# Optimization experiments

Measured on AMD Instinct MI355X. Metric: run time of the kernel, lower is better.

Reference implementation:

```python
import jax, jax.numpy as jnp
import numpy as np

N, E = 50000, 800000
IN_DIM, HID, H1, H2, NCLS = 512, 64, 4, 1, 40
NEG_SLOPE = 0.2


def gat_conv(x, src, dst, W, att_src, att_dst, b, heads, ch):
    # x: [N, F_in]; W: [F_in, heads*ch]; att_*: [heads, ch]; b: [heads*ch]
    n = x.shape[0]
    h = (x @ W).reshape(n, heads, ch)                      # [N,H,C]
    a_s = jnp.einsum('nhc,hc->nh', h, att_src)             # [N,H]
    a_d = jnp.einsum('nhc,hc->nh', h, att_dst)             # [N,H]
    e = jax.nn.leaky_relu(a_s[src] + a_d[dst], NEG_SLOPE)  # [E,H]
    # segment softmax over incoming edges of each destination node
    m = jax.ops.segment_max(e, dst, num_segments=n)        # [N,H]
    ex = jnp.exp(e - m[dst])
    s = jax.ops.segment_sum(ex, dst, num_segments=n)       # [N,H]
    alpha = ex / (s[dst] + 1e-16)                          # [E,H]
    out = jax.ops.segment_sum(alpha[:, :, None] * h[src], dst, num_segments=n)
    return out.reshape(n, heads * ch) + b


def setup_inputs() -> dict:
    key = jax.random.key(0)
    ks = jax.random.split(key, 10)
    glorot = lambda k, shp: jax.random.normal(k, shp, jnp.float32) * jnp.sqrt(2.0 / (shp[0] + shp[-1]))
    return {
        'x': jax.random.normal(ks[0], (N, IN_DIM), jnp.float32),
        'edge_index': jax.random.randint(ks[1], (2, E), 0, N, jnp.int64),
        'W1': glorot(ks[2], (IN_DIM, H1 * HID)),
        'att_src1': glorot(ks[3], (H1, HID)),
        'att_dst1': glorot(ks[4], (H1, HID)),
        'b1': jnp.zeros((H1 * HID,), jnp.float32),
        'W2': glorot(ks[5], (H1 * HID, H2 * NCLS)),
        'att_src2': glorot(ks[6], (H2, NCLS)),
        'att_dst2': glorot(ks[7], (H2, NCLS)),
        'b2': jnp.zeros((H2 * NCLS,), jnp.float32),
    }


def reference(x, edge_index, W1, att_src1, att_dst1, b1, W2, att_src2, att_dst2, b2):
    n = x.shape[0]
    loops = jnp.arange(n, dtype=edge_index.dtype)
    src = jnp.concatenate([edge_index[0], loops])  # add self loops (PyG default)
    dst = jnp.concatenate([edge_index[1], loops])
    # dropout layers are identity in eval mode
    h = gat_conv(x, src, dst, W1, att_src1, att_dst1, b1, H1, HID)
    h = jax.nn.elu(h)
    out = gat_conv(h, src, dst, W2, att_src2, att_dst2, b2, H2, NCLS)
    return jax.nn.log_softmax(out, axis=1)
```

## Files before the change

### kernel.cpp

```cpp
#include <hip/hip_runtime.h>
#include <math.h>
#include <stdint.h>


typedef short bf16x8 __attribute__((ext_vector_type(8)));
typedef float f32x4  __attribute__((ext_vector_type(4)));

static __device__ __forceinline__ float leaky(float x){ return x > 0.f ? x : 0.2f*x; }
static __device__ __forceinline__ unsigned short f2bf(float f){
  uint32_t u = __float_as_uint(f);
  uint32_t r = u + 0x7fffu + ((u >> 16) & 1u);
  return (unsigned short)(r >> 16);
}
static __device__ __forceinline__ float bf2f(unsigned short u){
  return __uint_as_float(((uint32_t)u) << 16);
}

__global__ void k_cvt_w(const float* __restrict__ W, unsigned short* __restrict__ wt,
                        int* __restrict__ deg, int n){
  int i = blockIdx.x*blockDim.x + threadIdx.x;
  if (i < n) deg[i] = 0;
  if (i >= 256*64) return;
  int col = i & 255, kg = i >> 8;
  int kt = kg >> 2, kq = kg & 3;
  unsigned short* dst = wt + ((size_t)kt*1024 + kq*256 + col)*8;
  bf16x8 p;
  #pragma unroll
  for (int j=0;j<8;j++) p[j] = (short)f2bf(W[(size_t)(kg*8+j)*256 + col]);
  *(bf16x8*)dst = p;
}

__global__ void k_count(const int* __restrict__ ei, int E, int n, int* __restrict__ deg){
  int i = blockIdx.x*blockDim.x + threadIdx.x;
  int tot = E + n;
  if (i >= tot) return;
  int dst = (i < E) ? ei[E + i] : (i - E);
  atomicAdd(&deg[dst], 1);
}

__global__ __launch_bounds__(256) void k_scan_a(const int* __restrict__ deg,
    int* __restrict__ rowstart, int* __restrict__ bsum, int n){
  __shared__ int sm[256];
  int b = blockIdx.x, t = threadIdx.x;
  int i = b*256 + t;
  int v = (i < n) ? deg[i] : 0;
  sm[t] = v;
  __syncthreads();
  for (int off=1; off<256; off<<=1){
    int u = (t >= off) ? sm[t-off] : 0;
    __syncthreads();
    sm[t] += u;
    __syncthreads();
  }
  if (i < n) rowstart[i+1] = sm[t];
  if (t == 255) bsum[b] = sm[255];
}
__global__ __launch_bounds__(256) void k_scan_b(int* __restrict__ bsum, int nb){
  __shared__ int sm[256];
  int t = threadIdx.x;
  int v = (t < nb) ? bsum[t] : 0;
  sm[t] = v;
  __syncthreads();
  for (int off=1; off<256; off<<=1){
    int u = (t >= off) ? sm[t-off] : 0;
    __syncthreads();
    sm[t] += u;
    __syncthreads();
  }
  if (t < nb) bsum[t] = sm[t] - v;
}
__global__ __launch_bounds__(256) void k_scan_c(int* __restrict__ rowstart,
    const int* __restrict__ bsum, int* __restrict__ cur, int n){
  int b = blockIdx.x, t = threadIdx.x;
  int i = b*256 + t;
  if (i < n){ rowstart[i+1] += bsum[b]; cur[i] = 0; }
  if (i == 0) rowstart[0] = 0;
}

__global__ __launch_bounds__(256, 4) void k_gemm1_mfma(const float* __restrict__ X,
                                                    const unsigned short* __restrict__ WT,
                                                    const float* __restrict__ SW,
                                                    const float* __restrict__ DW,
                                                    unsigned short* __restrict__ Cb,
                                                    float* __restrict__ as1,
                                                    float* __restrict__ ad1, int M){
  __shared__ __align__(16) unsigned short lA[2][2048];
  __shared__ __align__(16) unsigned short lB[2][4096];
  const int t = threadIdx.x;
  const int lane = t & 63, w = t >> 6;
  const int wx = w & 1, wy = w >> 1;
  const int row0 = blockIdx.x * 64, col0 = blockIdx.y * 128;

  f32x4 acc[2][4];
  #pragma unroll
  for (int i=0;i<2;i++)
    #pragma unroll
    for (int j=0;j<4;j++)
      #pragma unroll
      for (int r=0;r<4;r++) acc[i][j][r] = 0.f;

  const int rA = w*16 + (lane & 15);
  const int kA = lane >> 4;
  const float* xA = X + (size_t)min(row0 + rA, M-1)*512 + kA*8;
  const int aChunk = kA*64 + rA;

  const int c0 = t, c1 = t + 256;
  const unsigned short* bB0 = WT + ((size_t)(c0>>7)*256 + col0 + (c0&127))*8;
  const unsigned short* bB1 = WT + ((size_t)(c1>>7)*256 + col0 + (c1&127))*8;

  const int fkq = lane >> 4, li = lane & 15;

  float4 pA0, pA1, qA0, qA1;
  uint4  pB0, pB1, qB0, qB1;

#define LOAD_T(A0,A1,B0,B1, T) do{ \
  A0 = *(const float4*)(xA + (T)*32); \
  A1 = *(const float4*)(xA + (T)*32 + 4); \
  B0 = *(const uint4*)(bB0 + (size_t)(T)*8192); \
  B1 = *(const uint4*)(bB1 + (size_t)(T)*8192); }while(0)

#define WRITE_T(NXT, A0,A1,B0,B1) do{ \
  bf16x8 p0; \
  p0[0]=(short)f2bf(A0.x); p0[1]=(short)f2bf(A0.y); p0[2]=(short)f2bf(A0.z); p0[3]=(short)f2bf(A0.w); \
  p0[4]=(short)f2bf(A1.x); p0[5]=(short)f2bf(A1.y); p0[6]=(short)f2bf(A1.z); p0[7]=(short)f2bf(A1.w); \
  *(bf16x8*)&lA[NXT][aChunk*8] = p0; \
  *(uint4*)&lB[NXT][c0*8] = B0; \
  *(uint4*)&lB[NXT][c1*8] = B1; }while(0)

#define BARRIER() do{ \
  asm volatile("s_waitcnt lgkmcnt(0)" ::: "memory"); \
  __builtin_amdgcn_s_barrier(); \
  asm volatile("" ::: "memory"); }while(0)

#define STEP(T, CUR, A0,A1,B0,B1) do{ \
  bf16x8 af[2], bfr[4]; \
  _Pragma("unroll") \
  for (int i=0;i<2;i++) \
    af[i]  = *(const bf16x8*)&lA[CUR][(fkq*64 + wx*32 + i*16 + li)*8]; \
  _Pragma("unroll") \
  for (int j=0;j<4;j++) \
    bfr[j] = *(const bf16x8*)&lB[CUR][(fkq*128 + wy*64 + j*16 + li)*8]; \
  _Pragma("unroll") \
  for (int i=0;i<2;i++) \
    _Pragma("unroll") \
    for (int j=0;j<4;j++) \
      acc[i][j] = __builtin_amdgcn_mfma_f32_16x16x32_bf16(af[i], bfr[j], acc[i][j], 0, 0, 0); \
  if ((T) < 15){ \
    WRITE_T((CUR)^1, A0,A1,B0,B1); \
    if ((T) <= 12) LOAD_T(A0,A1,B0,B1, (T)+3); \
    BARRIER(); \
  } \
}while(0)

  {
    LOAD_T(pA0,pA1,pB0,pB1, 0);
    WRITE_T(0, pA0,pA1,pB0,pB1);
    LOAD_T(pA0,pA1,pB0,pB1, 1);
    LOAD_T(qA0,qA1,qB0,qB1, 2);
    BARRIER();
  }

  #pragma unroll
  for (int tt = 0; tt < 8; ++tt){
    STEP(2*tt,   (0), pA0,pA1,pB0,pB1);
    STEP(2*tt+1, (1), qA0,qA1,qB0,qB1);
  }

#undef STEP
#undef BARRIER
#undef WRITE_T
#undef LOAD_T

  #pragma unroll
  for (int i=0;i<2;i++){
    #pragma unroll
    for (int r=0;r<4;r++){
      int row = row0 + wx*32 + i*16 + fkq*4 + r;
      if (row < M){
        #pragma unroll
        for (int j=0;j<4;j++)
          Cb[(size_t)row*256 + col0 + wy*64 + j*16 + li] = f2bf(acc[i][j][r]);
      }
    }
  }

  const int hw = (int)blockIdx.y*2 + wy;
  float sv[4], dv[4];
  #pragma unroll
  for (int j=0;j<4;j++){
    sv[j] = SW[hw*64 + j*16 + li];
    dv[j] = DW[hw*64 + j*16 + li];
  }
  #pragma unroll
  for (int i=0;i<2;i++){
    #pragma unroll
    for (int r=0;r<4;r++){
      float ps = acc[i][0][r]*sv[0] + acc[i][1][r]*sv[1] + acc[i][2][r]*sv[2] + acc[i][3][r]*sv[3];
      float pd = acc[i][0][r]*dv[0] + acc[i][1][r]*dv[1] + acc[i][2][r]*dv[2] + acc[i][3][r]*dv[3];
      #pragma unroll
      for (int o=1;o<16;o<<=1){ ps += __shfl_xor(ps,o); pd += __shfl_xor(pd,o); }
      int row = row0 + wx*32 + i*16 + fkq*4 + r;
      if (li == 0 && row < M){
        as1[row*4 + hw] = ps;
        ad1[row*4 + hw] = pd;
      }
    }
  }
}

__global__ void k_fill(const int* __restrict__ ei, int E, int n,
                       const int* __restrict__ rowstart, int* __restrict__ cur,
                       int* __restrict__ csr,
                       const float* __restrict__ as1, const float* __restrict__ ad1,
                       float* __restrict__ exbuf){
  int i = blockIdx.x*blockDim.x + threadIdx.x;
  int tot = E + n;
  if (i >= tot) return;
  int src, dst;
  if (i < E){ src = ei[i]; dst = ei[E+i]; } else { src = i - E; dst = src; }
  int pos = atomicAdd(&cur[dst], 1);
  int slot = rowstart[dst] + pos;
  csr[slot] = src;
  float4 a = *(const float4*)(as1 + (size_t)src*4);
  float4 d = *(const float4*)(ad1 + (size_t)dst*4);
  float4 ex;
  ex.x = __expf(fminf(leaky(a.x + d.x), 80.f));
  ex.y = __expf(fminf(leaky(a.y + d.y), 80.f));
  ex.z = __expf(fminf(leaky(a.z + d.z), 80.f));
  ex.w = __expf(fminf(leaky(a.w + d.w), 80.f));
  *(float4*)(exbuf + (size_t)slot*4) = ex;
}

__global__ __launch_bounds__(256) void k_agg1(const unsigned short* __restrict__ h1b,
    const float* __restrict__ exbuf,
    const int* __restrict__ rowstart, const int* __restrict__ csr,
    const float* __restrict__ b1, unsigned short* __restrict__ hactb, int n){
  int lane = threadIdx.x & 63;
  int node = blockIdx.x*4 + (threadIdx.x >> 6);
  if (node >= n) return;
  int lo = __builtin_amdgcn_readfirstlane(rowstart[node]);
  int hi = __builtin_amdgcn_readfirstlane(rowstart[node+1]);
  int h = lane >> 4;
  const float* exb = exbuf + h;
  float ax=0.f, ay=0.f, az=0.f, aw=0.f, psum=0.f;
  int e = lo;
  for (; e + 7 < hi; e += 8){
    int s0 = csr[e],   s1 = csr[e+1], s2 = csr[e+2], s3 = csr[e+3];
    int s4 = csr[e+4], s5 = csr[e+5], s6 = csr[e+6], s7 = csr[e+7];
    float e0 = exb[(size_t)e*4],     e1 = exb[(size_t)(e+1)*4],
          e2 = exb[(size_t)(e+2)*4], e3 = exb[(size_t)(e+3)*4],
          e4 = exb[(size_t)(e+4)*4], e5 = exb[(size_t)(e+5)*4],
          e6 = exb[(size_t)(e+6)*4], e7 = exb[(size_t)(e+7)*4];
    ushort4 u0 = *(const ushort4*)(h1b + (size_t)s0*256 + lane*4);
    ushort4 u1 = *(const ushort4*)(h1b + (size_t)s1*256 + lane*4);
    ushort4 u2 = *(const ushort4*)(h1b + (size_t)s2*256 + lane*4);
    ushort4 u3 = *(const ushort4*)(h1b + (size_t)s3*256 + lane*4);
    ushort4 u4 = *(const ushort4*)(h1b + (size_t)s4*256 + lane*4);
    ushort4 u5 = *(const ushort4*)(h1b + (size_t)s5*256 + lane*4);
    ushort4 u6 = *(const ushort4*)(h1b + (size_t)s6*256 + lane*4);
    ushort4 u7 = *(const ushort4*)(h1b + (size_t)s7*256 + lane*4);
    ax += e0*bf2f(u0.x) + e1*bf2f(u1.x) + e2*bf2f(u2.x) + e3*bf2f(u3.x)
        + e4*bf2f(u4.x) + e5*bf2f(u5.x) + e6*bf2f(u6.x) + e7*bf2f(u7.x);
    ay += e0*bf2f(u0.y) + e1*bf2f(u1.y) + e2*bf2f(u2.y) + e3*bf2f(u3.y)
        + e4*bf2f(u4.y) + e5*bf2f(u5.y) + e6*bf2f(u6.y) + e7*bf2f(u7.y);
    az += e0*bf2f(u0.z) + e1*bf2f(u1.z) + e2*bf2f(u2.z) + e3*bf2f(u3.z)
        + e4*bf2f(u4.z) + e5*bf2f(u5.z) + e6*bf2f(u6.z) + e7*bf2f(u7.z);
    aw += e0*bf2f(u0.w) + e1*bf2f(u1.w) + e2*bf2f(u2.w) + e3*bf2f(u3.w)
        + e4*bf2f(u4.w) + e5*bf2f(u5.w) + e6*bf2f(u6.w) + e7*bf2f(u7.w);
    psum += (e0+e1+e2+e3) + (e4+e5+e6+e7);
  }
  for (; e < hi; ++e){
    int s0 = csr[e];
    float e0 = exb[(size_t)e*4];
    ushort4 u0 = *(const ushort4*)(h1b + (size_t)s0*256 + lane*4);
    ax += e0*bf2f(u0.x); ay += e0*bf2f(u0.y); az += e0*bf2f(u0.z); aw += e0*bf2f(u0.w);
    psum += e0;
  }
  float inv = 1.f/(psum + 1e-16f);
  float4 bv = *(const float4*)(b1 + lane*4);
  float o0 = ax*inv + bv.x, o1 = ay*inv + bv.y, o2 = az*inv + bv.z, o3 = aw*inv + bv.w;
  ushort4 r;
  r.x = f2bf(o0 > 0.f ? o0 : expm1f(o0));
  r.y = f2bf(o1 > 0.f ? o1 : expm1f(o1));
  r.z = f2bf(o2 > 0.f ? o2 : expm1f(o2));
  r.w = f2bf(o3 > 0.f ? o3 : expm1f(o3));
  *(ushort4*)(hactb + (size_t)node*256 + lane*4) = r;
}

__global__ __launch_bounds__(256) void k_gemm2(const unsigned short* __restrict__ A,
    const float* __restrict__ B, const float* __restrict__ sw, const float* __restrict__ dw,
    unsigned short* __restrict__ Cb, float* __restrict__ as2, float* __restrict__ ad2, int M){
  __shared__ float Xl[32][129];
  __shared__ float Wl[128*40];
  __shared__ float Sps[32][8], Spd[32][8];
  int t = threadIdx.x;
  int row0 = blockIdx.x*32;
  int r = t & 31, g = t >> 5;
  float acc[5] = {0,0,0,0,0};
  for (int kt=0; kt<256; kt+=128){
    for (int i=t; i<1280; i+=256)
      *(float4*)&Wl[i*4] = *(const float4*)(B + kt*40 + i*4);
    for (int i=t; i<512; i+=256){
      int rr = i >> 4, k8 = i & 15;
      int grow = row0 + rr; if (grow >= M) grow = M-1;
      uint4 v = *(const uint4*)(A + (size_t)grow*256 + kt + k8*8);
      float* xp = &Xl[rr][k8*8];
      xp[0] = __uint_as_float(v.x << 16); xp[1] = __uint_as_float(v.x & 0xffff0000u);
      xp[2] = __uint_as_float(v.y << 16); xp[3] = __uint_as_float(v.y & 0xffff0000u);
      xp[4] = __uint_as_float(v.z << 16); xp[5] = __uint_as_float(v.z & 0xffff0000u);
      xp[6] = __uint_as_float(v.w << 16); xp[7] = __uint_as_float(v.w & 0xffff0000u);
    }
    __syncthreads();
    #pragma unroll 4
    for (int k=0;k<128;++k){
      float a = Xl[r][k];
      const float* wp = &Wl[k*40 + g*5];
      #pragma unroll
      for (int j=0;j<5;++j) acc[j] += a * wp[j];
    }
    __syncthreads();
  }
  int grow = row0 + r;
  float ps = 0.f, pd = 0.f;
  #pragma unroll
  for (int j=0;j<5;++j){
    ps += acc[j] * sw[g*5+j];
    pd += acc[j] * dw[g*5+j];
  }
  Sps[r][g] = ps; Spd[r][g] = pd;
  if (grow < M){
    #pragma unroll
    for (int j=0;j<5;++j) Cb[(size_t)grow*40 + g*5 + j] = f2bf(acc[j]);
  }
  __syncthreads();
  if (t < 32){
    float a = 0.f, b = 0.f;
    #pragma unroll
    for (int g2=0; g2<8; ++g2){ a += Sps[t][g2]; b += Spd[t][g2]; }
    int rw = row0 + t;
    if (rw < M){ as2[rw] = a; ad2[rw] = b; }
  }
}

__global__ __launch_bounds__(256) void k_pre2(const float* __restrict__ as2,
    const float* __restrict__ ad2, const int* __restrict__ rowstart,
    const int* __restrict__ csr, float* __restrict__ ex2, int n){
  int lane = threadIdx.x & 63;
  int node = blockIdx.x*4 + (threadIdx.x >> 6);
  if (node >= n) return;
  int lo = rowstart[node], hi = rowstart[node+1];
  float adn = ad2[node];
  for (int e = lo + lane; e < hi; e += 64)
    ex2[e] = __expf(fminf(leaky(as2[csr[e]] + adn), 80.f));
}

__global__ __launch_bounds__(256) void k_agg2(const unsigned short* __restrict__ h2b,
    const float* __restrict__ ex2,
    const int* __restrict__ rowstart, const int* __restrict__ csr,
    const float* __restrict__ b2, float* __restrict__ out, int n){
  int lane = threadIdx.x & 63;
  int node = blockIdx.x*4 + (threadIdx.x >> 6);
  if (node >= n) return;
  int lo = __builtin_amdgcn_readfirstlane(rowstart[node]);
  int hi = __builtin_amdgcn_readfirstlane(rowstart[node+1]);
  bool act = lane < 40;
  float acc = 0.f, psum = 0.f;
  int e = lo;
  for (; e + 7 < hi; e += 8){
    int s0 = csr[e],   s1 = csr[e+1], s2 = csr[e+2], s3 = csr[e+3];
    int s4 = csr[e+4], s5 = csr[e+5], s6 = csr[e+6], s7 = csr[e+7];
    float e0 = ex2[e],   e1 = ex2[e+1], e2 = ex2[e+2], e3 = ex2[e+3];
    float e4 = ex2[e+4], e5 = ex2[e+5], e6 = ex2[e+6], e7 = ex2[e+7];
    float h0 = act ? bf2f(h2b[(size_t)s0*40 + lane]) : 0.f;
    float h1 = act ? bf2f(h2b[(size_t)s1*40 + lane]) : 0.f;
    float h2 = act ? bf2f(h2b[(size_t)s2*40 + lane]) : 0.f;
    float h3 = act ? bf2f(h2b[(size_t)s3*40 + lane]) : 0.f;
    float h4 = act ? bf2f(h2b[(size_t)s4*40 + lane]) : 0.f;
    float h5 = act ? bf2f(h2b[(size_t)s5*40 + lane]) : 0.f;
    float h6 = act ? bf2f(h2b[(size_t)s6*40 + lane]) : 0.f;
    float h7 = act ? bf2f(h2b[(size_t)s7*40 + lane]) : 0.f;
    acc += e0*h0 + e1*h1 + e2*h2 + e3*h3 + e4*h4 + e5*h5 + e6*h6 + e7*h7;
    psum += (e0+e1+e2+e3) + (e4+e5+e6+e7);
  }
  for (; e < hi; ++e){
    int s0 = csr[e]; float e0 = ex2[e];
    acc += e0 * (act ? bf2f(h2b[(size_t)s0*40 + lane]) : 0.f);
    psum += e0;
  }
  float ov = acc/(psum + 1e-16f) + (act ? b2[lane] : 0.f);
  float v = act ? ov : -INFINITY;
  float mx = v;
  #pragma unroll
  for (int o=1;o<64;o<<=1) mx = fmaxf(mx, __shfl_xor(mx,o));
  float ev = act ? __expf(ov - mx) : 0.f;
  float se = ev;
  #pragma unroll
  for (int o=1;o<64;o<<=1) se += __shfl_xor(se,o);
  if (act) out[(size_t)node*40 + lane] = (ov - mx) - __logf(se);
}

extern "C" void kernel_launch(void* const* d_in, const int* in_sizes, int n_in,
                              void* d_out, int out_size, void* d_ws, size_t ws_size,
                              hipStream_t stream){
  const float* x   = (const float*)d_in[0];
  const int*   ei  = (const int*)d_in[1];
  const float* W1  = (const float*)d_in[2];
  const float* s1w = (const float*)d_in[3];
  const float* d1w = (const float*)d_in[4];
  const float* b1  = (const float*)d_in[5];
  const float* W2  = (const float*)d_in[6];
  const float* s2w = (const float*)d_in[7];
  const float* d2w = (const float*)d_in[8];
  const float* b2  = (const float*)d_in[9];
  float* out = (float*)d_out;

  const int N  = in_sizes[0] / 512;
  const int E  = in_sizes[1] / 2;
  const int Et = E + N;

  float* f = (float*)d_ws;
  unsigned short* h1b   = (unsigned short*)f;  f += (size_t)N*128;
  unsigned short* hactb = (unsigned short*)f;  f += (size_t)N*128;
  float* as1  = f;  f += (size_t)N*4;
  float* ad1  = f;  f += (size_t)N*4;
  float* as2  = f;  f += N;
  float* ad2  = f;  f += N;
  unsigned short* w1t = (unsigned short*)f;  f += 256*512/2;
  unsigned short* h2b = (unsigned short*)f;  f += (size_t)N*40/2 + 64;
  float* exbuf = f;  f += (size_t)Et*4;
  float* ex2   = f;  f += Et;
  int* ip = (int*)f;
  int* rowstart = ip;  ip += (N + 4) & ~3;
  int* deg      = ip;  ip += N;
  int* cur      = ip;  ip += N;
  int* csr      = ip;  ip += Et;
  int* bsum     = ip;  ip += 256;

  int nb4 = (N + 3) / 4;
  int nbs = (N + 255) / 256;
  k_cvt_w<<<nbs, 256, 0, stream>>>(W1, w1t, deg, N);
  k_count<<<(Et+255)/256, 256, 0, stream>>>(ei, E, N, deg);
  k_scan_a<<<nbs, 256, 0, stream>>>(deg, rowstart, bsum, N);
  k_scan_b<<<1, 256, 0, stream>>>(bsum, nbs);
  k_scan_c<<<nbs, 256, 0, stream>>>(rowstart, bsum, cur, N);
  k_gemm1_mfma<<<dim3((N+63)/64, 2), 256, 0, stream>>>(x, w1t, s1w, d1w, h1b, as1, ad1, N);
  k_fill <<<(Et+255)/256, 256, 0, stream>>>(ei, E, N, rowstart, cur, csr, as1, ad1, exbuf);
  k_agg1 <<<nb4, 256, 0, stream>>>(h1b, exbuf, rowstart, csr, b1, hactb, N);
  k_gemm2<<<(N+31)/32, 256, 0, stream>>>(hactb, W2, s2w, d2w, h2b, as2, ad2, N);
  k_pre2 <<<nb4, 256, 0, stream>>>(as2, ad2, rowstart, csr, ex2, N);
  k_agg2 <<<nb4, 256, 0, stream>>>(h2b, ex2, rowstart, csr, b2, out, N);
}
```

Measured before the change: 455.3 us.

## Use MFMA for layer-2 GEMM, fuse edge softmax into agg2, single-kernel scan

Replaces the scalar FP32 second-layer GEMM with a bf16 MFMA kernel that reads a pre-converted, padded W2 prepared in the weight-conversion kernel. The separate pre2 edge-exponent pass is dropped, and agg2 now computes the attention exponent inline from as2/ad2, which removes the ex2 buffer write and read. The three-kernel degree scan is collapsed into a single 1024-thread block scan to cut launches. The trade-offs are extra exp work per gathered edge, a serial per-thread segment in the single-block scan, and lower precision on W2.

```diff
diff --git a/kernel.cpp b/kernel.cpp
--- a/kernel.cpp
+++ b/kernel.cpp
@@ -17,17 +17,27 @@
 }
 
 __global__ void k_cvt_w(const float* __restrict__ W, unsigned short* __restrict__ wt,
+                        const float* __restrict__ W2, unsigned short* __restrict__ wt2,
                         int* __restrict__ deg, int n){
   int i = blockIdx.x*blockDim.x + threadIdx.x;
   if (i < n) deg[i] = 0;
-  if (i >= 256*64) return;
-  int col = i & 255, kg = i >> 8;
-  int kt = kg >> 2, kq = kg & 3;
-  unsigned short* dst = wt + ((size_t)kt*1024 + kq*256 + col)*8;
-  bf16x8 p;
-  #pragma unroll
-  for (int j=0;j<8;j++) p[j] = (short)f2bf(W[(size_t)(kg*8+j)*256 + col]);
-  *(bf16x8*)dst = p;
+  if (i < 256*64){
+    int col = i & 255, kg = i >> 8;
+    int kt = kg >> 2, kq = kg & 3;
+    unsigned short* dst = wt + ((size_t)kt*1024 + kq*256 + col)*8;
+    bf16x8 p;
+    #pragma unroll
+    for (int j=0;j<8;j++) p[j] = (short)f2bf(W[(size_t)(kg*8+j)*256 + col]);
+    *(bf16x8*)dst = p;
+  } else if (i < 256*64 + 2048) {
+    int i2 = i - 256*64;
+    int col = i2 & 63, kg = i2 >> 6;
+    bf16x8 p;
+    #pragma unroll
+    for (int j=0;j<8;j++)
+      p[j] = (col < 40) ? (short)f2bf(W2[(size_t)(kg*8+j)*40 + col]) : (short)0;
+    *(bf16x8*)(wt2 + (size_t)i2*8) = p;
+  }
 }
 
 __global__ void k_count(const int* __restrict__ ei, int E, int n, int* __restrict__ deg){
@@ -38,43 +48,28 @@
   atomicAdd(&deg[dst], 1);
 }
 
-__global__ __launch_bounds__(256) void k_scan_a(const int* __restrict__ deg,
-    int* __restrict__ rowstart, int* __restrict__ bsum, int n){
-  __shared__ int sm[256];
-  int b = blockIdx.x, t = threadIdx.x;
-  int i = b*256 + t;
-  int v = (i < n) ? deg[i] : 0;
-  sm[t] = v;
+__global__ __launch_bounds__(1024) void k_scan_one(const int* __restrict__ deg,
+    int* __restrict__ rowstart, int* __restrict__ cur, int n){
+  __shared__ int sm[1024];
+  int t = threadIdx.x;
+  const int per = (n + 1023) / 1024;
+  int base = t * per;
+  int s = 0;
+  for (int i=0;i<per;i++){ int idx = base+i; if (idx < n) s += deg[idx]; }
+  sm[t] = s;
   __syncthreads();
-  for (int off=1; off<256; off<<=1){
+  for (int off=1; off<1024; off<<=1){
     int u = (t >= off) ? sm[t-off] : 0;
     __syncthreads();
     sm[t] += u;
     __syncthreads();
   }
-  if (i < n) rowstart[i+1] = sm[t];
-  if (t == 255) bsum[b] = sm[255];
-}
-__global__ __launch_bounds__(256) void k_scan_b(int* __restrict__ bsum, int nb){
-  __shared__ int sm[256];
-  int t = threadIdx.x;
-  int v = (t < nb) ? bsum[t] : 0;
-  sm[t] = v;
-  __syncthreads();
-  for (int off=1; off<256; off<<=1){
-    int u = (t >= off) ? sm[t-off] : 0;
-    __syncthreads();
-    sm[t] += u;
-    __syncthreads();
-  }
-  if (t < nb) bsum[t] = sm[t] - v;
-}
-__global__ __launch_bounds__(256) void k_scan_c(int* __restrict__ rowstart,
-    const int* __restrict__ bsum, int* __restrict__ cur, int n){
-  int b = blockIdx.x, t = threadIdx.x;
-  int i = b*256 + t;
-  if (i < n){ rowstart[i+1] += bsum[b]; cur[i] = 0; }
-  if (i == 0) rowstart[0] = 0;
+  int r = sm[t] - s;
+  for (int i=0;i<per;i++){
+    int idx = base+i;
+    if (idx < n){ r += deg[idx]; rowstart[idx+1] = r; cur[idx] = 0; }
+  }
+  if (t == 0) rowstart[0] = 0;
 }
 
 __global__ __launch_bounds__(256, 4) void k_gemm1_mfma(const float* __restrict__ X,
@@ -287,75 +282,107 @@
   *(ushort4*)(hactb + (size_t)node*256 + lane*4) = r;
 }
 
-__global__ __launch_bounds__(256) void k_gemm2(const unsigned short* __restrict__ A,
-    const float* __restrict__ B, const float* __restrict__ sw, const float* __restrict__ dw,
-    unsigned short* __restrict__ Cb, float* __restrict__ as2, float* __restrict__ ad2, int M){
-  __shared__ float Xl[32][129];
-  __shared__ float Wl[128*40];
-  __shared__ float Sps[32][8], Spd[32][8];
-  int t = threadIdx.x;
-  int row0 = blockIdx.x*32;
-  int r = t & 31, g = t >> 5;
-  float acc[5] = {0,0,0,0,0};
-  for (int kt=0; kt<256; kt+=128){
-    for (int i=t; i<1280; i+=256)
-      *(float4*)&Wl[i*4] = *(const float4*)(B + kt*40 + i*4);
-    for (int i=t; i<512; i+=256){
-      int rr = i >> 4, k8 = i & 15;
-      int grow = row0 + rr; if (grow >= M) grow = M-1;
-      uint4 v = *(const uint4*)(A + (size_t)grow*256 + kt + k8*8);
-      float* xp = &Xl[rr][k8*8];
-      xp[0] = __uint_as_float(v.x << 16); xp[1] = __uint_as_float(v.x & 0xffff0000u);
-      xp[2] = __uint_as_float(v.y << 16); xp[3] = __uint_as_float(v.y & 0xffff0000u);
-      xp[4] = __uint_as_float(v.z << 16); xp[5] = __uint_as_float(v.z & 0xffff0000u);
-      xp[6] = __uint_as_float(v.w << 16); xp[7] = __uint_as_float(v.w & 0xffff0000u);
+__global__ __launch_bounds__(256, 4) void k_gemm2_mfma(const unsigned short* __restrict__ A,
+    const unsigned short* __restrict__ WT2, const float* __restrict__ sw,
+    const float* __restrict__ dw, unsigned short* __restrict__ Cb,
+    float* __restrict__ as2, float* __restrict__ ad2, int M){
+  __shared__ __align__(16) unsigned short lA[2][2048];
+  __shared__ __align__(16) unsigned short lB[2][2048];
+  const int t = threadIdx.x;
+  const int lane = t & 63, w = t >> 6;
+  const int row0 = blockIdx.x * 64;
+
+  f32x4 acc[4];
+  #pragma unroll
+  for (int j=0;j<4;j++)
+    #pragma unroll
+    for (int r=0;r<4;r++) acc[j][r] = 0.f;
+
+  const int rA = w*16 + (lane & 15);
+  const int kA = lane >> 4;
+  const unsigned short* pA = A + (size_t)min(row0 + rA, M-1)*256 + kA*8;
+  const int aChunk = kA*64 + rA;
+  const unsigned short* pB = WT2 + (size_t)t*8;
+
+  const int fkq = lane >> 4, li = lane & 15;
+
+  uint4 pAv, pBv, qAv, qBv;
+
+#define LOAD_T(AV,BV, T) do{ \
+  AV = *(const uint4*)(pA + (T)*32); \
+  BV = *(const uint4*)(pB + (size_t)(T)*2048); }while(0)
+
+#define WRITE_T(NXT, AV,BV) do{ \
+  *(uint4*)&lA[NXT][aChunk*8] = AV; \
+  *(uint4*)&lB[NXT][t*8] = BV; }while(0)
+
+#define BARRIER() do{ \
+  asm volatile("s_waitcnt lgkmcnt(0)" ::: "memory"); \
+  __builtin_amdgcn_s_barrier(); \
+  asm volatile("" ::: "memory"); }while(0)
+
+#define STEP(T, CUR, AV,BV) do{ \
+  bf16x8 af = *(const bf16x8*)&lA[CUR][(fkq*64 + w*16 + li)*8]; \
+  bf16x8 bfr[4]; \
+  _Pragma("unroll") \
+  for (int j=0;j<4;j++) \
+    bfr[j] = *(const bf16x8*)&lB[CUR][(fkq*64 + j*16 + li)*8]; \
+  _Pragma("unroll") \
+  for (int j=0;j<4;j++) \
+    acc[j] = __builtin_amdgcn_mfma_f32_16x16x32_bf16(af, bfr[j], acc[j], 0, 0, 0); \
+  if ((T) < 7){ \
+    WRITE_T((CUR)^1, AV,BV); \
+    if ((T) <= 4) LOAD_T(AV,BV, (T)+3); \
+    BARRIER(); \
+  } \
+}while(0)
+
+  {
+    LOAD_T(pAv,pBv, 0);
+    WRITE_T(0, pAv,pBv);
+    LOAD_T(pAv,pBv, 1);
+    LOAD_T(qAv,qBv, 2);
+    BARRIER();
+  }
+  STEP(0, 0, pAv,pBv);
+  STEP(1, 1, qAv,qBv);
+  STEP(2, 0, pAv,pBv);
+  STEP(3, 1, qAv,qBv);
+  STEP(4, 0, pAv,pBv);
+  STEP(5, 1, qAv,qBv);
+  STEP(6, 0, pAv,pBv);
+  STEP(7, 1, qAv,qBv);
+
+#undef STEP
+#undef BARRIER
+#undef WRITE_T
+#undef LOAD_T
+
+  float swv[4], dwv[4];
+  #pragma unroll
+  for (int j=0;j<4;j++){
+    int col = j*16 + li;
+    swv[j] = (col < 40) ? sw[col] : 0.f;
+    dwv[j] = (col < 40) ? dw[col] : 0.f;
+  }
+  #pragma unroll
+  for (int r=0;r<4;r++){
+    int grow = row0 + w*16 + fkq*4 + r;
+    if (grow < M){
+      Cb[(size_t)grow*40 + li]      = f2bf(acc[0][r]);
+      Cb[(size_t)grow*40 + 16 + li] = f2bf(acc[1][r]);
+      if (li < 8) Cb[(size_t)grow*40 + 32 + li] = f2bf(acc[2][r]);
     }
-    __syncthreads();
-    #pragma unroll 4
-    for (int k=0;k<128;++k){
-      float a = Xl[r][k];
-      const float* wp = &Wl[k*40 + g*5];
-      #pragma unroll
-      for (int j=0;j<5;++j) acc[j] += a * wp[j];
-    }
-    __syncthreads();
-  }
-  int grow = row0 + r;
-  float ps = 0.f, pd = 0.f;
-  #pragma unroll
-  for (int j=0;j<5;++j){
-    ps += acc[j] * sw[g*5+j];
-    pd += acc[j] * dw[g*5+j];
-  }
-  Sps[r][g] = ps; Spd[r][g] = pd;
-  if (grow < M){
-    #pragma unroll
-    for (int j=0;j<5;++j) Cb[(size_t)grow*40 + g*5 + j] = f2bf(acc[j]);
-  }
-  __syncthreads();
-  if (t < 32){
-    float a = 0.f, b = 0.f;
-    #pragma unroll
-    for (int g2=0; g2<8; ++g2){ a += Sps[t][g2]; b += Spd[t][g2]; }
-    int rw = row0 + t;
-    if (rw < M){ as2[rw] = a; ad2[rw] = b; }
-  }
-}
-
-__global__ __launch_bounds__(256) void k_pre2(const float* __restrict__ as2,
-    const float* __restrict__ ad2, const int* __restrict__ rowstart,
-    const int* __restrict__ csr, float* __restrict__ ex2, int n){
-  int lane = threadIdx.x & 63;
-  int node = blockIdx.x*4 + (threadIdx.x >> 6);
-  if (node >= n) return;
-  int lo = rowstart[node], hi = rowstart[node+1];
-  float adn = ad2[node];
-  for (int e = lo + lane; e < hi; e += 64)
-    ex2[e] = __expf(fminf(leaky(as2[csr[e]] + adn), 80.f));
+    float ps = acc[0][r]*swv[0] + acc[1][r]*swv[1] + acc[2][r]*swv[2] + acc[3][r]*swv[3];
+    float pd = acc[0][r]*dwv[0] + acc[1][r]*dwv[1] + acc[2][r]*dwv[2] + acc[3][r]*dwv[3];
+    #pragma unroll
+    for (int o=1;o<16;o<<=1){ ps += __shfl_xor(ps,o); pd += __shfl_xor(pd,o); }
+    if (li == 0 && grow < M){ as2[grow] = ps; ad2[grow] = pd; }
+  }
 }
 
 __global__ __launch_bounds__(256) void k_agg2(const unsigned short* __restrict__ h2b,
-    const float* __restrict__ ex2,
+    const float* __restrict__ as2, const float* __restrict__ ad2,
     const int* __restrict__ rowstart, const int* __restrict__ csr,
     const float* __restrict__ b2, float* __restrict__ out, int n){
   int lane = threadIdx.x & 63;
@@ -363,14 +390,21 @@
   if (node >= n) return;
   int lo = __builtin_amdgcn_readfirstlane(rowstart[node]);
   int hi = __builtin_amdgcn_readfirstlane(rowstart[node+1]);
+  float adn = ad2[node];
   bool act = lane < 40;
   float acc = 0.f, psum = 0.f;
   int e = lo;
   for (; e + 7 < hi; e += 8){
     int s0 = csr[e],   s1 = csr[e+1], s2 = csr[e+2], s3 = csr[e+3];
     int s4 = csr[e+4], s5 = csr[e+5], s6 = csr[e+6], s7 = csr[e+7];
-    float e0 = ex2[e],   e1 = ex2[e+1], e2 = ex2[e+2], e3 = ex2[e+3];
-    float e4 = ex2[e+4], e5 = ex2[e+5], e6 = ex2[e+6], e7 = ex2[e+7];
+    float e0 = __expf(fminf(leaky(as2[s0] + adn), 80.f));
+    float e1 = __expf(fminf(leaky(as2[s1] + adn), 80.f));
+    float e2 = __expf(fminf(leaky(as2[s2] + adn), 80.f));
+    float e3 = __expf(fminf(leaky(as2[s3] + adn), 80.f));
+    float e4 = __expf(fminf(leaky(as2[s4] + adn), 80.f));
+    float e5 = __expf(fminf(leaky(as2[s5] + adn), 80.f));
+    float e6 = __expf(fminf(leaky(as2[s6] + adn), 80.f));
+    float e7 = __expf(fminf(leaky(as2[s7] + adn), 80.f));
     float h0 = act ? bf2f(h2b[(size_t)s0*40 + lane]) : 0.f;
     float h1 = act ? bf2f(h2b[(size_t)s1*40 + lane]) : 0.f;
     float h2 = act ? bf2f(h2b[(size_t)s2*40 + lane]) : 0.f;
@@ -383,7 +417,8 @@
     psum += (e0+e1+e2+e3) + (e4+e5+e6+e7);
   }
   for (; e < hi; ++e){
-    int s0 = csr[e]; float e0 = ex2[e];
+    int s0 = csr[e];
+    float e0 = __expf(fminf(leaky(as2[s0] + adn), 80.f));
     acc += e0 * (act ? bf2f(h2b[(size_t)s0*40 + lane]) : 0.f);
     psum += e0;
   }
@@ -426,27 +461,23 @@
   float* as2  = f;  f += N;
   float* ad2  = f;  f += N;
   unsigned short* w1t = (unsigned short*)f;  f += 256*512/2;
+  unsigned short* w2t = (unsigned short*)f;  f += 2048*8/2;
   unsigned short* h2b = (unsigned short*)f;  f += (size_t)N*40/2 + 64;
   float* exbuf = f;  f += (size_t)Et*4;
-  float* ex2   = f;  f += Et;
   int* ip = (int*)f;
   int* rowstart = ip;  ip += (N + 4) & ~3;
   int* deg      = ip;  ip += N;
   int* cur      = ip;  ip += N;
   int* csr      = ip;  ip += Et;
-  int* bsum     = ip;  ip += 256;
 
   int nb4 = (N + 3) / 4;
   int nbs = (N + 255) / 256;
-  k_cvt_w<<<nbs, 256, 0, stream>>>(W1, w1t, deg, N);
+  k_cvt_w<<<nbs, 256, 0, stream>>>(W1, w1t, W2, w2t, deg, N);
   k_count<<<(Et+255)/256, 256, 0, stream>>>(ei, E, N, deg);
-  k_scan_a<<<nbs, 256, 0, stream>>>(deg, rowstart, bsum, N);
-  k_scan_b<<<1, 256, 0, stream>>>(bsum, nbs);
-  k_scan_c<<<nbs, 256, 0, stream>>>(rowstart, bsum, cur, N);
+  k_scan_one<<<1, 1024, 0, stream>>>(deg, rowstart, cur, N);
   k_gemm1_mfma<<<dim3((N+63)/64, 2), 256, 0, stream>>>(x, w1t, s1w, d1w, h1b, as1, ad1, N);
   k_fill <<<(Et+255)/256, 256, 0, stream>>>(ei, E, N, rowstart, cur, csr, as1, ad1, exbuf);
   k_agg1 <<<nb4, 256, 0, stream>>>(h1b, exbuf, rowstart, csr, b1, hactb, N);
-  k_gemm2<<<(N+31)/32, 256, 0, stream>>>(hactb, W2, s2w, d2w, h2b, as2, ad2, N);
-  k_pre2 <<<nb4, 256, 0, stream>>>(as2, ad2, rowstart, csr, ex2, N);
-  k_agg2 <<<nb4, 256, 0, stream>>>(h2b, ex2, rowstart, csr, b2, out, N);
-}
+  k_gemm2_mfma<<<(N+63)/64, 256, 0, stream>>>(hactb, w2t, s2w, d2w, h2b, as2, ad2, N);
+  k_agg2 <<<nb4, 256, 0, stream>>>(h2b, as2, ad2, rowstart, csr, b2, out, N);
+}
```

New measurement: 526.1 us. 1.16x slower.
